# Performance work log

Measured on AMD Instinct MI355X. Metric: run time of the kernel, lower is better.

Reference implementation:

```python
import jax, jax.numpy as jnp
import numpy as np

N_NODES = 100000
N_EDGES = 1600000
D_IN = 64
D_OUT = 64


def setup_inputs() -> dict:
    key = jax.random.key(0)
    k1, k2, k3, k4 = jax.random.split(key, 4)
    feat = jax.random.normal(k1, (N_NODES, D_IN), dtype=jnp.float32)
    edge_src = jax.random.randint(k2, (N_EDGES,), 0, N_NODES, dtype=jnp.int64)
    edge_dst = jax.random.randint(k3, (N_EDGES,), 0, N_NODES, dtype=jnp.int64)
    # xavier_uniform with gain for relu (sqrt(2)) on [out, in] Linear weight
    gain = float(np.sqrt(2.0))
    limit = gain * float(np.sqrt(6.0 / (D_IN + D_OUT)))
    fc_weight = jax.random.uniform(k4, (D_OUT, D_IN), dtype=jnp.float32,
                                   minval=-limit, maxval=limit)
    return {"feat": feat, "edge_src": edge_src, "edge_dst": edge_dst,
            "fc_weight": fc_weight}


def reference(feat, edge_src, edge_dst, fc_weight):
    # SDDMM: edge score a_e = <h_src, h_dst>  (fn.u_dot_v)
    h_src = feat[edge_src]                      # [E, d]
    h_dst = feat[edge_dst]                      # [E, d]
    a = jnp.sum(h_src * h_dst, axis=-1, keepdims=True)  # [E, 1]
    # SpMM: neigh[v] = sum_{(u->v)} h_u * a_e  (u_mul_e + sum)
    m = h_src * a                               # [E, d]
    neigh = jax.ops.segment_sum(m, edge_dst, num_segments=feat.shape[0])  # [N, d]
    # Linear without bias: y = neigh @ W.T
    return neigh @ fc_weight.T
```

## Files before the change

kernel.cpp:

```cpp
#include <hip/hip_runtime.h>

#define N_NODES 100000
#define N_EDGES 1600000
#define D 64
#define NB 782
#define CAP 3072
#define EPB 8192
#define NPART ((N_EDGES + EPB - 1) / EPB)
#define RSH 14

typedef unsigned short ushort_t;
typedef unsigned int uint_t;

__device__ __forceinline__ ushort_t f2bf(float f) {
    uint_t u = __float_as_uint(f);
    u += 0x7FFF + ((u >> 16) & 1);
    return (ushort_t)(u >> 16);
}

__global__ __launch_bounds__(256) void repack_init(const float* __restrict__ feat,
                                                   ushort_t* __restrict__ featb,
                                                   int* __restrict__ gcur) {
    const int tid = blockIdx.x * 256 + threadIdx.x;
    if (tid < NB) gcur[tid] = tid * CAP;
    const int base = tid * 16;
    if (base >= N_NODES * D) return;
    const float4* f4 = (const float4*)(feat + base);
    ushort4* o4 = (ushort4*)(featb + base);
#pragma unroll
    for (int j = 0; j < 4; ++j) {
        const float4 v = f4[j];
        o4[j] = make_ushort4(f2bf(v.x), f2bf(v.y), f2bf(v.z), f2bf(v.w));
    }
}

__global__ __launch_bounds__(1024) void partition(const int* __restrict__ esrc,
                                                  const int* __restrict__ edst,
                                                  int* __restrict__ gcur,
                                                  int* __restrict__ slab) {
    __shared__ int stage[EPB];
    __shared__ ushort_t bkt16[EPB];
    __shared__ int cnt[NB];
    __shared__ int cur[NB];
    __shared__ int gb[NB];
    __shared__ int s[1024];
    const int t = threadIdx.x;
    const int base = blockIdx.x * EPB;
    const int n = min(EPB, N_EDGES - base);

    if (t < NB) cnt[t] = 0;
    __syncthreads();
    for (int i = t; i < n; i += 1024)
        atomicAdd(&cnt[edst[base + i] >> 7], 1);
    __syncthreads();
    const int v = (t < NB) ? cnt[t] : 0;
    s[t] = v;
    __syncthreads();
    for (int off = 1; off < 1024; off <<= 1) {
        const int x = (t >= off) ? s[t - off] : 0;
        __syncthreads();
        s[t] += x;
        __syncthreads();
    }
    if (t < NB) {
        const int excl = s[t] - v;
        cur[t] = excl;
        gb[t] = (v ? atomicAdd(&gcur[t], v) : 0) - excl;
    }
    __syncthreads();
    for (int i = t; i < n; i += 1024) {
        const int d = edst[base + i];
        const int bkt = d >> 7;
        const int pos = atomicAdd(&cur[bkt], 1);
        stage[pos] = ((d & 127) << 17) | esrc[base + i];
        bkt16[pos] = (ushort_t)bkt;
    }
    __syncthreads();
    for (int i = t; i < n; i += 1024) {
        const int bkt = bkt16[i];
        const int gp = gb[bkt] + i;
        if (gp < (bkt + 1) * CAP)
            slab[gp] = stage[i];
    }
}

template<int CTRL>
__device__ __forceinline__ float fadd_dpp(float x) {
    const int r = __builtin_amdgcn_update_dpp(0, __float_as_int(x), CTRL, 0xF, 0xF, true);
    return x + __int_as_float(r);
}
__device__ __forceinline__ float red8(float p) {
    p = fadd_dpp<0xB1>(p);
    p = fadd_dpp<0x4E>(p);
    p = fadd_dpp<0x141>(p);
    return p;
}

__device__ __forceinline__ float cvt_dot(const uint4 u, const float* __restrict__ h,
                                         float* __restrict__ g) {
    g[0] = __uint_as_float(u.x << 16); g[1] = __uint_as_float(u.x & 0xFFFF0000u);
    g[2] = __uint_as_float(u.y << 16); g[3] = __uint_as_float(u.y & 0xFFFF0000u);
    g[4] = __uint_as_float(u.z << 16); g[5] = __uint_as_float(u.z & 0xFFFF0000u);
    g[6] = __uint_as_float(u.w << 16); g[7] = __uint_as_float(u.w & 0xFFFF0000u);
    float p = 0.f;
#pragma unroll
    for (int k = 0; k < 8; ++k) p += g[k] * h[k];
    return p;
}

__global__ __launch_bounds__(512) void fused_spmm(const float4* __restrict__ feat4,
                                                  const uint4* __restrict__ featb4,
                                                  const int* __restrict__ slab,
                                                  const int* __restrict__ gcur,
                                                  float4* __restrict__ neigh4) {
    __shared__ int seA[CAP];
    __shared__ int seB[CAP];
    __shared__ int cnt[1024];
    __shared__ int cur[1024];
    __shared__ int rowoff[129];
    __shared__ int s[512];
    const int t = threadIdx.x;
    const int b = blockIdx.x;
    const int nbase = b << 7;
    const int nb_nodes = min(128, N_NODES - nbase);
    const int sbase = b * CAP;
    const int ne = min(gcur[b] - sbase, CAP);

    for (int i = t; i < ne; i += 512) seA[i] = slab[sbase + i];
    cnt[t] = 0; cnt[t + 512] = 0;
    __syncthreads();
    for (int i = t; i < ne; i += 512) {
        const int pk = seA[i];
        atomicAdd(&cnt[((pk >> 17) << 3) | ((pk & 0x1FFFF) >> RSH)], 1);
    }
    __syncthreads();
    const int v0 = cnt[2 * t], v1 = cnt[2 * t + 1];
    const int sum = v0 + v1;
    s[t] = sum;
    __syncthreads();
    for (int off = 1; off < 512; off <<= 1) {
        const int x = (t >= off) ? s[t - off] : 0;
        __syncthreads();
        s[t] += x;
        __syncthreads();
    }
    const int excl = s[t] - sum;
    cur[2 * t] = excl;
    cur[2 * t + 1] = excl + v0;
    __syncthreads();
    if (t < 128) rowoff[t] = cur[t << 3];
    if (t == 0) rowoff[128] = ne;
    __syncthreads();
    for (int i = t; i < ne; i += 512) {
        const int pk = seA[i];
        const int key = ((pk >> 17) << 3) | ((pk & 0x1FFFF) >> RSH);
        const int pos = atomicAdd(&cur[key], 1);
        seB[pos] = pk & 0x1FFFF;
    }
    __syncthreads();

    const int slot = t >> 3;
    const int l = t & 7;
#pragma unroll
    for (int ln0 = 0; ln0 < 128; ln0 += 64) {
        const int ln = ln0 + slot;
        if (ln >= nb_nodes) continue;
        const int nidx = nbase + ln;
        float h[8];
        {
            const float4 ha = feat4[nidx * 16 + 2 * l];
            const float4 hb = feat4[nidx * 16 + 2 * l + 1];
            h[0] = ha.x; h[1] = ha.y; h[2] = ha.z; h[3] = ha.w;
            h[4] = hb.x; h[5] = hb.y; h[6] = hb.z; h[7] = hb.w;
        }
        float acc[8];
#pragma unroll
        for (int k = 0; k < 8; ++k) acc[k] = 0.f;

        int e = rowoff[ln];
        const int e1 = rowoff[ln + 1];
        for (; e + 3 < e1; e += 4) {
            const int s0 = seB[e], s1 = seB[e + 1], s2 = seB[e + 2], s3 = seB[e + 3];
            const uint4 u0 = featb4[s0 * 8 + l];
            const uint4 u1 = featb4[s1 * 8 + l];
            const uint4 u2 = featb4[s2 * 8 + l];
            const uint4 u3 = featb4[s3 * 8 + l];
            float g0[8], g1[8], g2[8], g3[8];
            float p0 = cvt_dot(u0, h, g0);
            float p1 = cvt_dot(u1, h, g1);
            float p2 = cvt_dot(u2, h, g2);
            float p3 = cvt_dot(u3, h, g3);
            p0 = red8(p0); p1 = red8(p1); p2 = red8(p2); p3 = red8(p3);
#pragma unroll
            for (int k = 0; k < 8; ++k)
                acc[k] += g0[k] * p0 + g1[k] * p1 + g2[k] * p2 + g3[k] * p3;
        }
        for (; e < e1; ++e) {
            const uint4 u0 = featb4[seB[e] * 8 + l];
            float g0[8];
            float p0 = red8(cvt_dot(u0, h, g0));
#pragma unroll
            for (int k = 0; k < 8; ++k) acc[k] += g0[k] * p0;
        }
        neigh4[nidx * 16 + 2 * l]     = make_float4(acc[0], acc[1], acc[2], acc[3]);
        neigh4[nidx * 16 + 2 * l + 1] = make_float4(acc[4], acc[5], acc[6], acc[7]);
    }
}

__global__ __launch_bounds__(256) void gemm_inplace(float* __restrict__ out,
                                                    const float* __restrict__ W) {
    __shared__ float WT[64][68];
    __shared__ float nT[64][132];
    const int t = threadIdx.x;

    const float4* W4 = (const float4*)W;
#pragma unroll
    for (int j = 0; j < 4; ++j) {
        const int f = t + j * 256;
        const int o = f >> 4;
        const int i4 = (f & 15) * 4;
        const float4 w = W4[f];
        WT[i4 + 0][o] = w.x;
        WT[i4 + 1][o] = w.y;
        WT[i4 + 2][o] = w.z;
        WT[i4 + 3][o] = w.w;
    }

    const int base = blockIdx.x * 128;
    const int rows = min(128, N_NODES - base);
    const float4* O4 = (const float4*)(out + (long)base * D);
#pragma unroll
    for (int j = 0; j < 8; ++j) {
        const int f = t + j * 256;
        const int r = f >> 4;
        const int i4 = (f & 15) * 4;
        if (r < rows) {
            const float4 x = O4[f];
            nT[i4 + 0][r] = x.x;
            nT[i4 + 1][r] = x.y;
            nT[i4 + 2][r] = x.z;
            nT[i4 + 3][r] = x.w;
        }
    }
    __syncthreads();

    const int c4 = (t & 15) * 4;
    const int r0 = (t >> 4) * 8;
    float acc[8][4];
#pragma unroll
    for (int r = 0; r < 8; ++r)
#pragma unroll
        for (int c = 0; c < 4; ++c) acc[r][c] = 0.f;

    for (int i = 0; i < 64; ++i) {
        const float4 w = *(const float4*)&WT[i][c4];
        const float4 ra = *(const float4*)&nT[i][r0];
        const float4 rb = *(const float4*)&nT[i][r0 + 4];
        const float wv[4] = {w.x, w.y, w.z, w.w};
        const float rv[8] = {ra.x, ra.y, ra.z, ra.w, rb.x, rb.y, rb.z, rb.w};
#pragma unroll
        for (int r = 0; r < 8; ++r)
#pragma unroll
            for (int c = 0; c < 4; ++c) acc[r][c] += rv[r] * wv[c];
    }

#pragma unroll
    for (int r = 0; r < 8; ++r) {
        const int rr = r0 + r;
        if (rr < rows)
            *(float4*)&out[(long)(base + rr) * D + c4] =
                make_float4(acc[r][0], acc[r][1], acc[r][2], acc[r][3]);
    }
}

extern "C" void kernel_launch(void* const* d_in, const int* in_sizes, int n_in,
                              void* d_out, int out_size, void* d_ws, size_t ws_size,
                              hipStream_t stream) {
    const float* feat = (const float*)d_in[0];
    const int*   esrc = (const int*)d_in[1];
    const int*   edst = (const int*)d_in[2];
    const float* W    = (const float*)d_in[3];
    float* out = (float*)d_out;

    char* ws = (char*)d_ws;
    ushort_t* featb = (ushort_t*)(ws);
    int* slab = (int*)(ws + 12800000);
    int* gcur = (int*)(ws + 12800000 + (size_t)NB * CAP * 4);

    repack_init<<<(N_NODES * D / 16 + 255) / 256, 256, 0, stream>>>(feat, featb, gcur);
    partition<<<NPART, 1024, 0, stream>>>(esrc, edst, gcur, slab);
    fused_spmm<<<NB, 512, 0, stream>>>((const float4*)feat, (const uint4*)featb,
                                       slab, gcur, (float4*)out);
    gemm_inplace<<<(N_NODES + 127) / 128, 256, 0, stream>>>(out, W);
}
```

Measured before the change: 168.9 us.

## Fuse dense linear projection into SpMM kernel via shared-memory accumulator tile

Each aggregation block now writes its 128x64 neighbour sums into a shared-memory tile that overlays the edge-sorting scratch buffers. The same block then multiplies that tile by W in-register and writes the final output. This removes the separate GEMM launch and the round trip of the intermediate through global memory. The destination node's own features are now read from the bf16 copy instead of fp32, which lowers precision in the dot product. The extra 64-float wcol array per thread may raise register pressure in a 512-thread block.

```diff
diff --git a/kernel.cpp b/kernel.cpp
--- a/kernel.cpp
+++ b/kernel.cpp
@@ -96,29 +96,38 @@
     return p;
 }
 
-__device__ __forceinline__ float cvt_dot(const uint4 u, const float* __restrict__ h,
-                                         float* __restrict__ g) {
+__device__ __forceinline__ void cvt8(const uint4 u, float* __restrict__ g) {
     g[0] = __uint_as_float(u.x << 16); g[1] = __uint_as_float(u.x & 0xFFFF0000u);
     g[2] = __uint_as_float(u.y << 16); g[3] = __uint_as_float(u.y & 0xFFFF0000u);
     g[4] = __uint_as_float(u.z << 16); g[5] = __uint_as_float(u.z & 0xFFFF0000u);
     g[6] = __uint_as_float(u.w << 16); g[7] = __uint_as_float(u.w & 0xFFFF0000u);
+}
+__device__ __forceinline__ float cvt_dot(const uint4 u, const float* __restrict__ h,
+                                         float* __restrict__ g) {
+    cvt8(u, g);
     float p = 0.f;
 #pragma unroll
     for (int k = 0; k < 8; ++k) p += g[k] * h[k];
     return p;
 }
 
-__global__ __launch_bounds__(512) void fused_spmm(const float4* __restrict__ feat4,
-                                                  const uint4* __restrict__ featb4,
-                                                  const int* __restrict__ slab,
-                                                  const int* __restrict__ gcur,
-                                                  float4* __restrict__ neigh4) {
-    __shared__ int seA[CAP];
+__global__ __launch_bounds__(512) void fused_spmm_gemm(
+    const uint4* __restrict__ featb4,
+    const int* __restrict__ slab,
+    const int* __restrict__ gcur,
+    const float* __restrict__ W,
+    float* __restrict__ out)
+{
+    __shared__ __align__(16) char ovl[32768];
     __shared__ int seB[CAP];
-    __shared__ int cnt[1024];
-    __shared__ int cur[1024];
     __shared__ int rowoff[129];
-    __shared__ int s[512];
+    int* seA     = (int*)ovl;
+    int* kcnt    = (int*)(ovl + 12288);
+    int* kcur    = (int*)(ovl + 16384);
+    int* s       = (int*)(ovl + 20480);
+    float* accs  = (float*)ovl;
+    float4* accs4 = (float4*)ovl;
+
     const int t = threadIdx.x;
     const int b = blockIdx.x;
     const int nbase = b << 7;
@@ -127,14 +136,14 @@
     const int ne = min(gcur[b] - sbase, CAP);
 
     for (int i = t; i < ne; i += 512) seA[i] = slab[sbase + i];
-    cnt[t] = 0; cnt[t + 512] = 0;
+    kcnt[t] = 0; kcnt[t + 512] = 0;
     __syncthreads();
     for (int i = t; i < ne; i += 512) {
         const int pk = seA[i];
-        atomicAdd(&cnt[((pk >> 17) << 3) | ((pk & 0x1FFFF) >> RSH)], 1);
-    }
-    __syncthreads();
-    const int v0 = cnt[2 * t], v1 = cnt[2 * t + 1];
+        atomicAdd(&kcnt[((pk >> 17) << 3) | ((pk & 0x1FFFF) >> RSH)], 1);
+    }
+    __syncthreads();
+    const int v0 = kcnt[2 * t], v1 = kcnt[2 * t + 1];
     const int sum = v0 + v1;
     s[t] = sum;
     __syncthreads();
@@ -145,16 +154,16 @@
         __syncthreads();
     }
     const int excl = s[t] - sum;
-    cur[2 * t] = excl;
-    cur[2 * t + 1] = excl + v0;
-    __syncthreads();
-    if (t < 128) rowoff[t] = cur[t << 3];
+    kcur[2 * t] = excl;
+    kcur[2 * t + 1] = excl + v0;
+    __syncthreads();
+    if (t < 128) rowoff[t] = kcur[t << 3];
     if (t == 0) rowoff[128] = ne;
     __syncthreads();
     for (int i = t; i < ne; i += 512) {
         const int pk = seA[i];
         const int key = ((pk >> 17) << 3) | ((pk & 0x1FFFF) >> RSH);
-        const int pos = atomicAdd(&cur[key], 1);
+        const int pos = atomicAdd(&kcur[key], 1);
         seB[pos] = pk & 0x1FFFF;
     }
     __syncthreads();
@@ -167,12 +176,7 @@
         if (ln >= nb_nodes) continue;
         const int nidx = nbase + ln;
         float h[8];
-        {
-            const float4 ha = feat4[nidx * 16 + 2 * l];
-            const float4 hb = feat4[nidx * 16 + 2 * l + 1];
-            h[0] = ha.x; h[1] = ha.y; h[2] = ha.z; h[3] = ha.w;
-            h[4] = hb.x; h[5] = hb.y; h[6] = hb.z; h[7] = hb.w;
-        }
+        cvt8(featb4[nidx * 8 + l], h);
         float acc[8];
 #pragma unroll
         for (int k = 0; k < 8; ++k) acc[k] = 0.f;
@@ -202,74 +206,35 @@
 #pragma unroll
             for (int k = 0; k < 8; ++k) acc[k] += g0[k] * p0;
         }
-        neigh4[nidx * 16 + 2 * l]     = make_float4(acc[0], acc[1], acc[2], acc[3]);
-        neigh4[nidx * 16 + 2 * l + 1] = make_float4(acc[4], acc[5], acc[6], acc[7]);
-    }
-}
-
-__global__ __launch_bounds__(256) void gemm_inplace(float* __restrict__ out,
-                                                    const float* __restrict__ W) {
-    __shared__ float WT[64][68];
-    __shared__ float nT[64][132];
-    const int t = threadIdx.x;
-
-    const float4* W4 = (const float4*)W;
-#pragma unroll
-    for (int j = 0; j < 4; ++j) {
-        const int f = t + j * 256;
-        const int o = f >> 4;
-        const int i4 = (f & 15) * 4;
-        const float4 w = W4[f];
-        WT[i4 + 0][o] = w.x;
-        WT[i4 + 1][o] = w.y;
-        WT[i4 + 2][o] = w.z;
-        WT[i4 + 3][o] = w.w;
-    }
-
-    const int base = blockIdx.x * 128;
-    const int rows = min(128, N_NODES - base);
-    const float4* O4 = (const float4*)(out + (long)base * D);
-#pragma unroll
-    for (int j = 0; j < 8; ++j) {
-        const int f = t + j * 256;
-        const int r = f >> 4;
-        const int i4 = (f & 15) * 4;
-        if (r < rows) {
-            const float4 x = O4[f];
-            nT[i4 + 0][r] = x.x;
-            nT[i4 + 1][r] = x.y;
-            nT[i4 + 2][r] = x.z;
-            nT[i4 + 3][r] = x.w;
-        }
-    }
-    __syncthreads();
-
-    const int c4 = (t & 15) * 4;
-    const int r0 = (t >> 4) * 8;
-    float acc[8][4];
-#pragma unroll
-    for (int r = 0; r < 8; ++r)
-#pragma unroll
-        for (int c = 0; c < 4; ++c) acc[r][c] = 0.f;
-
-    for (int i = 0; i < 64; ++i) {
-        const float4 w = *(const float4*)&WT[i][c4];
-        const float4 ra = *(const float4*)&nT[i][r0];
-        const float4 rb = *(const float4*)&nT[i][r0 + 4];
-        const float wv[4] = {w.x, w.y, w.z, w.w};
-        const float rv[8] = {ra.x, ra.y, ra.z, ra.w, rb.x, rb.y, rb.z, rb.w};
-#pragma unroll
-        for (int r = 0; r < 8; ++r)
-#pragma unroll
-            for (int c = 0; c < 4; ++c) acc[r][c] += rv[r] * wv[c];
-    }
-
-#pragma unroll
-    for (int r = 0; r < 8; ++r) {
-        const int rr = r0 + r;
-        if (rr < rows)
-            *(float4*)&out[(long)(base + rr) * D + c4] =
-                make_float4(acc[r][0], acc[r][1], acc[r][2], acc[r][3]);
+        accs4[ln * 16 + 2 * l]     = make_float4(acc[0], acc[1], acc[2], acc[3]);
+        accs4[ln * 16 + 2 * l + 1] = make_float4(acc[4], acc[5], acc[6], acc[7]);
+    }
+    __syncthreads();
+
+    const int o = t & 63;
+    const int rg = t >> 6;
+    float wcol[D];
+    {
+        const float4* W4 = (const float4*)(W + o * D);
+#pragma unroll
+        for (int i4 = 0; i4 < 16; ++i4) {
+            const float4 w = W4[i4];
+            wcol[4 * i4 + 0] = w.x; wcol[4 * i4 + 1] = w.y;
+            wcol[4 * i4 + 2] = w.z; wcol[4 * i4 + 3] = w.w;
+        }
+    }
+    for (int r = rg; r < nb_nodes; r += 8) {
+        const float4* arow = (const float4*)&accs[r * D];
+        float sumv = 0.f;
+#pragma unroll
+        for (int i4 = 0; i4 < 16; ++i4) {
+            const float4 a4 = arow[i4];
+            sumv += a4.x * wcol[4 * i4 + 0];
+            sumv += a4.y * wcol[4 * i4 + 1];
+            sumv += a4.z * wcol[4 * i4 + 2];
+            sumv += a4.w * wcol[4 * i4 + 3];
+        }
+        out[(nbase + r) * D + o] = sumv;
     }
 }
 
@@ -289,7 +254,5 @@
 
     repack_init<<<(N_NODES * D / 16 + 255) / 256, 256, 0, stream>>>(feat, featb, gcur);
     partition<<<NPART, 1024, 0, stream>>>(esrc, edst, gcur, slab);
-    fused_spmm<<<NB, 512, 0, stream>>>((const float4*)feat, (const uint4*)featb,
-                                       slab, gcur, (float4*)out);
-    gemm_inplace<<<(N_NODES + 127) / 128, 256, 0, stream>>>(out, W);
-}
+    fused_spmm_gemm<<<NB, 512, 0, stream>>>((const uint4*)featb, slab, gcur, W, out);
+}
```

Measured after the change: 203.0 us. 1.2x slower.
